# Kernel tuning notes

Hardware: AMD Instinct MI355X
Metric: run time of the kernel (lower is better)

The kernel has to match this reference:

```python
import jax, jax.numpy as jnp
import numpy as np

H = 256
B = 2048
T = 512


def setup_inputs() -> dict:
    key = jax.random.key(0)
    k0, k1, k2, k3, k4 = jax.random.split(key, 5)
    s = 1.0 / np.sqrt(H)  # PyTorch LSTMCell init bound
    return {
        "h": jax.random.normal(k0, (B, H), jnp.float32),
        "W_ih": jax.random.uniform(k1, (4 * H, H), jnp.float32, -s, s),
        "W_hh": jax.random.uniform(k2, (4 * H, H), jnp.float32, -s, s),
        "b_ih": jax.random.uniform(k3, (4 * H,), jnp.float32, -s, s),
        "b_hh": jax.random.uniform(k4, (4 * H,), jnp.float32, -s, s),
        "sequence_length": T,
    }


def _lstm_cell(x, h, c, W_ih, W_hh, b_ih, b_hh):
    # PyTorch LSTMCell: gates ordered (i, f, g, o)
    gates = x @ W_ih.T + h @ W_hh.T + (b_ih + b_hh)  # [B, 4H]
    i, f, g, o = jnp.split(gates, 4, axis=-1)
    i = jax.nn.sigmoid(i)
    f = jax.nn.sigmoid(f)
    g = jnp.tanh(g)
    o = jax.nn.sigmoid(o)
    c2 = f * c + i * g
    h2 = o * jnp.tanh(c2)
    return h2, c2


def reference(h, W_ih, W_hh, b_ih, b_hh, sequence_length):
    b = h.shape[0]
    hid = W_hh.shape[1]
    z = jnp.zeros((b, hid), h.dtype)
    # t == 0: cell(h) with default zero hidden state
    h0, c0 = _lstm_cell(h, z, z, W_ih, W_hh, b_ih, b_hh)

    # t >= 1: input to the cell is the previous hidden output h (linear is None)
    def step(carry, _):
        hh, cc = carry
        h2, c2 = _lstm_cell(hh, hh, cc, W_ih, W_hh, b_ih, b_hh)
        return (h2, c2), h2

    (hf, cf), hs = jax.lax.scan(step, (h0, c0), None, length=sequence_length - 1)
    hs_all = jnp.concatenate([h0[None], hs], axis=0)  # [T, B, H], forward time order
    # predict_backward=True writes x_hat[-t] = h_t, so index 0 stays, rest reversed
    x_hat = jnp.concatenate([hs_all[:1], hs_all[1:][::-1]], axis=0)
    return x_hat, hf, cf
```

## Files before the change

### kernel.cpp

```cpp
#include <hip/hip_runtime.h>

#define HID   256
#define BATCH 2048
#define NGATE 1024
#define BM    16
#define NWG   128
#define TPB   1024
#define LDS_BYTES 147456

typedef __attribute__((ext_vector_type(8))) short bf16x8;
typedef __attribute__((ext_vector_type(4))) float f32x4;

__device__ __forceinline__ unsigned short f2bf(float x){
  unsigned int u = __builtin_bit_cast(unsigned int, x);
  u += 0x7fffu + ((u >> 16) & 1u);
  return (unsigned short)(u >> 16);
}
__device__ __forceinline__ float fsigm(float x){
  return __builtin_amdgcn_rcpf(1.0f + __expf(-x));
}
__device__ __forceinline__ float ftanh_(float x){
  return fmaf(2.0f, __builtin_amdgcn_rcpf(1.0f + __expf(-2.0f*x)), -1.0f);
}

__global__ void pack_kernel(const float* __restrict__ Wih, const float* __restrict__ Whh,
                            const float* __restrict__ bih, const float* __restrict__ bhh,
                            unsigned short* __restrict__ Wih_p,
                            unsigned short* __restrict__ Wsum_p,
                            float* __restrict__ bias){
  int tid = blockIdx.x * blockDim.x + threadIdx.x;
  int j  = tid & 7;
  int ln = (tid >> 3) & 63;
  int kt = (tid >> 9) & 7;
  int nt = tid >> 12;
  int n = nt*16 + (ln & 15);
  int k = kt*32 + (ln >> 4)*8 + j;
  float wih = Wih[n*HID + k];
  float whh = Whh[n*HID + k];
  Wih_p[tid]  = f2bf(wih);
  Wsum_p[tid] = f2bf(wih + whh);
  if (tid < NGATE) bias[tid] = bih[tid] + bhh[tid];
}

template<bool FIRST>
__device__ __forceinline__ void lstm_step(
    int t, int T, int g, int w, int l, int l15, int lq,
    const unsigned short* __restrict__ hcur,
    unsigned short* __restrict__ hnext,
    const unsigned short* __restrict__ wl,
    const bf16x8 (&wregs)[4][4],
    const unsigned short* __restrict__ Wih_p,
    const unsigned short* __restrict__ Wsum_p,
    const float (&bv)[4], float (&cs)[4],
    float* __restrict__ out)
{
  const f32x4 z = {0.f,0.f,0.f,0.f};
  f32x4 acc[4] = {z,z,z,z};

  if constexpr (FIRST){
    #pragma unroll
    for (int kt = 0; kt < 8; ++kt){
      bf16x8 av = *(const bf16x8*)&hcur[kt*512 + l*8];
      #pragma unroll
      for (int ga = 0; ga < 4; ++ga){
        bf16x8 bfr = *(const bf16x8*)(Wih_p + (size_t)((ga*16 + w)*8 + kt)*512 + l*8);
        acc[ga] = __builtin_amdgcn_mfma_f32_16x16x32_bf16(av, bfr, acc[ga], 0, 0, 0);
      }
    }
  } else {
    bf16x8 bs[4][2];
    #pragma unroll
    for (int ks = 0; ks < 2; ++ks)
      #pragma unroll
      for (int ga = 0; ga < 4; ++ga)
        bs[ga][ks] = *(const bf16x8*)(Wsum_p + (size_t)((ga*16 + w)*8 + 6 + ks)*512 + l*8);
    __builtin_amdgcn_sched_barrier(0);

    #pragma unroll
    for (int kc = 0; kc < 4; ++kc){
      bf16x8 av = *(const bf16x8*)&hcur[kc*512 + l*8];
      #pragma unroll
      for (int ga = 0; ga < 4; ++ga)
        acc[ga] = __builtin_amdgcn_mfma_f32_16x16x32_bf16(av, wregs[ga][kc], acc[ga], 0, 0, 0);
    }

    #pragma unroll
    for (int kc = 0; kc < 2; ++kc){
      bf16x8 av = *(const bf16x8*)&hcur[(4+kc)*512 + l*8];
      #pragma unroll
      for (int ga = 0; ga < 4; ++ga){
        bf16x8 bfr = *(const bf16x8*)&wl[((w*8) + ga*2 + kc)*512 + l*8];
        acc[ga] = __builtin_amdgcn_mfma_f32_16x16x32_bf16(av, bfr, acc[ga], 0, 0, 0);
      }
    }

    #pragma unroll
    for (int ks = 0; ks < 2; ++ks){
      bf16x8 av = *(const bf16x8*)&hcur[(6+ks)*512 + l*8];
      #pragma unroll
      for (int ga = 0; ga < 4; ++ga)
        acc[ga] = __builtin_amdgcn_mfma_f32_16x16x32_bf16(av, bs[ga][ks], acc[ga], 0, 0, 0);
    }
  }

  const int u   = w*16 + l15;
  const int ktu = w >> 1;
  const int kgu = ((w & 1) << 1) | (l15 >> 3);
  const int ju  = l15 & 7;
  const int orow = FIRST ? 0 : (T - t);
  float* __restrict__ orp = out + (size_t)orow * (BATCH*HID);
  const bool last = (t == T - 1);

  #pragma unroll
  for (int r = 0; r < 4; ++r){
    const int m = lq*4 + r;
    const float iv = fsigm (acc[0][r] + bv[0]);
    const float fv = fsigm (acc[1][r] + bv[1]);
    const float gv = ftanh_(acc[2][r] + bv[2]);
    const float ov = fsigm (acc[3][r] + bv[3]);
    const float cn = fv * cs[r] + iv * gv;
    cs[r] = cn;
    const float hv = ov * ftanh_(cn);
    hnext[ktu*512 + (kgu*16 + m)*8 + ju] = f2bf(hv);
    const size_t gi = (size_t)(g*BM + m)*HID + u;
    orp[gi] = hv;
    if (last){
      out[(size_t)T*(BATCH*HID) + gi]       = hv;
      out[(size_t)(T + 1)*(BATCH*HID) + gi] = cn;
    }
  }
}

__global__ __launch_bounds__(TPB, 4)
void lstm_kernel(const float* __restrict__ h_in,
                 const unsigned short* __restrict__ Wih_p,
                 const unsigned short* __restrict__ Wsum_p,
                 const float* __restrict__ bias,
                 const int* __restrict__ seqlen,
                 float* __restrict__ out){
  extern __shared__ unsigned short lds[];
  unsigned short* hb = lds;
  unsigned short* wl = lds + 8192;

  const int T   = seqlen[0];
  const int g   = blockIdx.x;
  const int tid = threadIdx.x;
  const int w   = tid >> 6;
  const int l   = tid & 63;
  const int l15 = l & 15;
  const int lq  = l >> 4;
  const int u   = w*16 + l15;

  float bv[4];
  #pragma unroll
  for (int ga = 0; ga < 4; ++ga) bv[ga] = bias[ga*256 + u];

  bf16x8 wregs[4][4];
  #pragma unroll
  for (int ga = 0; ga < 4; ++ga)
    #pragma unroll
    for (int kc = 0; kc < 4; ++kc)
      wregs[ga][kc] = *(const bf16x8*)(Wsum_p + (size_t)((ga*16 + w)*8 + kc)*512 + l*8);

  #pragma unroll
  for (int ga = 0; ga < 4; ++ga)
    #pragma unroll
    for (int kc = 0; kc < 2; ++kc)
      *(bf16x8*)&wl[((w*8) + ga*2 + kc)*512 + l*8] =
        *(const bf16x8*)(Wsum_p + (size_t)((ga*16 + w)*8 + 4 + kc)*512 + l*8);

  {
    const int ktu = w >> 1;
    const int kgu = ((w & 1) << 1) | (l15 >> 3);
    const int ju  = l15 & 7;
    #pragma unroll
    for (int r = 0; r < 4; ++r){
      const int m = lq*4 + r;
      hb[ktu*512 + (kgu*16 + m)*8 + ju] = f2bf(h_in[(size_t)(g*BM + m)*HID + u]);
    }
  }

  float cs[4] = {0.f, 0.f, 0.f, 0.f};
  __syncthreads();

  lstm_step<true>(0, T, g, w, l, l15, lq, hb, hb + 4096, wl, wregs, Wih_p, Wsum_p, bv, cs, out);
  __syncthreads();
  int buf = 1;
  for (int t = 1; t < T; ++t){
    lstm_step<false>(t, T, g, w, l, l15, lq,
                     hb + buf*4096, hb + (buf^1)*4096, wl, wregs, Wih_p, Wsum_p, bv, cs, out);
    __syncthreads();
    buf ^= 1;
  }
}

extern "C" void kernel_launch(void* const* d_in, const int* in_sizes, int n_in,
                              void* d_out, int out_size, void* d_ws, size_t ws_size,
                              hipStream_t stream) {
  const float* h_in = (const float*)d_in[0];
  const float* Wih  = (const float*)d_in[1];
  const float* Whh  = (const float*)d_in[2];
  const float* bih  = (const float*)d_in[3];
  const float* bhh  = (const float*)d_in[4];
  const int*   seq  = (const int*)  d_in[5];
  float* out = (float*)d_out;

  unsigned short* Wih_p  = (unsigned short*)d_ws;
  unsigned short* Wsum_p = Wih_p + (size_t)NGATE * HID;
  float*          bias   = (float*)(Wsum_p + (size_t)NGATE * HID);

  static bool attr_set = false;
  if (!attr_set){
    hipFuncSetAttribute((const void*)lstm_kernel,
                        hipFuncAttributeMaxDynamicSharedMemorySize, LDS_BYTES);
    attr_set = true;
  }

  pack_kernel<<<dim3((NGATE*HID)/256), dim3(256), 0, stream>>>(
      Wih, Whh, bih, bhh, Wih_p, Wsum_p, bias);

  lstm_kernel<<<dim3(NWG), dim3(TPB), LDS_BYTES, stream>>>(
      h_in, Wih_p, Wsum_p, bias, seq, out);
}
```

Baseline: 2.690 ms.

## Halve workgroup to 8 waves, each computing two unit tiles with more register-resident weights

Workgroups shrink from 16 to 8 waves, and each wave now owns 32 hidden units (two 16-wide tiles) per gate. More of the summed weight matrix stays in VGPRs (28 fragments), a larger slice goes to LDS, and the rest is streamed from global memory in staged batches between MFMA groups. Bias is folded into the accumulator initialisation, and __syncthreads is replaced by an explicit lgkmcnt wait plus s_barrier. The aim is cheaper per-step barriers and fewer global weight reloads, at the cost of half as many waves to hide latency and higher register pressure.

```diff
diff --git a/kernel.cpp b/kernel.cpp
--- a/kernel.cpp
+++ b/kernel.cpp
@@ -5,8 +5,8 @@
 #define NGATE 1024
 #define BM    16
 #define NWG   128
-#define TPB   1024
-#define LDS_BYTES 147456
+#define TPB   512
+#define LDS_BYTES 163840
 
 typedef __attribute__((ext_vector_type(8))) short bf16x8;
 typedef __attribute__((ext_vector_type(4))) float f32x4;
@@ -22,6 +22,15 @@
 __device__ __forceinline__ float ftanh_(float x){
   return fmaf(2.0f, __builtin_amdgcn_rcpf(1.0f + __expf(-2.0f*x)), -1.0f);
 }
+
+#define MFMA(a,b,c) __builtin_amdgcn_mfma_f32_16x16x32_bf16((a),(b),(c),0,0,0)
+
+#define STEP_BARRIER() do {                                   \
+    __builtin_amdgcn_sched_barrier(0);                        \
+    asm volatile("s_waitcnt lgkmcnt(0)" ::: "memory");        \
+    __builtin_amdgcn_s_barrier();                             \
+    __builtin_amdgcn_sched_barrier(0);                        \
+  } while (0)
 
 __global__ void pack_kernel(const float* __restrict__ Wih, const float* __restrict__ Whh,
                             const float* __restrict__ bih, const float* __restrict__ bhh,
@@ -42,96 +51,7 @@
   if (tid < NGATE) bias[tid] = bih[tid] + bhh[tid];
 }
 
-template<bool FIRST>
-__device__ __forceinline__ void lstm_step(
-    int t, int T, int g, int w, int l, int l15, int lq,
-    const unsigned short* __restrict__ hcur,
-    unsigned short* __restrict__ hnext,
-    const unsigned short* __restrict__ wl,
-    const bf16x8 (&wregs)[4][4],
-    const unsigned short* __restrict__ Wih_p,
-    const unsigned short* __restrict__ Wsum_p,
-    const float (&bv)[4], float (&cs)[4],
-    float* __restrict__ out)
-{
-  const f32x4 z = {0.f,0.f,0.f,0.f};
-  f32x4 acc[4] = {z,z,z,z};
-
-  if constexpr (FIRST){
-    #pragma unroll
-    for (int kt = 0; kt < 8; ++kt){
-      bf16x8 av = *(const bf16x8*)&hcur[kt*512 + l*8];
-      #pragma unroll
-      for (int ga = 0; ga < 4; ++ga){
-        bf16x8 bfr = *(const bf16x8*)(Wih_p + (size_t)((ga*16 + w)*8 + kt)*512 + l*8);
-        acc[ga] = __builtin_amdgcn_mfma_f32_16x16x32_bf16(av, bfr, acc[ga], 0, 0, 0);
-      }
-    }
-  } else {
-    bf16x8 bs[4][2];
-    #pragma unroll
-    for (int ks = 0; ks < 2; ++ks)
-      #pragma unroll
-      for (int ga = 0; ga < 4; ++ga)
-        bs[ga][ks] = *(const bf16x8*)(Wsum_p + (size_t)((ga*16 + w)*8 + 6 + ks)*512 + l*8);
-    __builtin_amdgcn_sched_barrier(0);
-
-    #pragma unroll
-    for (int kc = 0; kc < 4; ++kc){
-      bf16x8 av = *(const bf16x8*)&hcur[kc*512 + l*8];
-      #pragma unroll
-      for (int ga = 0; ga < 4; ++ga)
-        acc[ga] = __builtin_amdgcn_mfma_f32_16x16x32_bf16(av, wregs[ga][kc], acc[ga], 0, 0, 0);
-    }
-
-    #pragma unroll
-    for (int kc = 0; kc < 2; ++kc){
-      bf16x8 av = *(const bf16x8*)&hcur[(4+kc)*512 + l*8];
-      #pragma unroll
-      for (int ga = 0; ga < 4; ++ga){
-        bf16x8 bfr = *(const bf16x8*)&wl[((w*8) + ga*2 + kc)*512 + l*8];
-        acc[ga] = __builtin_amdgcn_mfma_f32_16x16x32_bf16(av, bfr, acc[ga], 0, 0, 0);
-      }
-    }
-
-    #pragma unroll
-    for (int ks = 0; ks < 2; ++ks){
-      bf16x8 av = *(const bf16x8*)&hcur[(6+ks)*512 + l*8];
-      #pragma unroll
-      for (int ga = 0; ga < 4; ++ga)
-        acc[ga] = __builtin_amdgcn_mfma_f32_16x16x32_bf16(av, bs[ga][ks], acc[ga], 0, 0, 0);
-    }
-  }
-
-  const int u   = w*16 + l15;
-  const int ktu = w >> 1;
-  const int kgu = ((w & 1) << 1) | (l15 >> 3);
-  const int ju  = l15 & 7;
-  const int orow = FIRST ? 0 : (T - t);
-  float* __restrict__ orp = out + (size_t)orow * (BATCH*HID);
-  const bool last = (t == T - 1);
-
-  #pragma unroll
-  for (int r = 0; r < 4; ++r){
-    const int m = lq*4 + r;
-    const float iv = fsigm (acc[0][r] + bv[0]);
-    const float fv = fsigm (acc[1][r] + bv[1]);
-    const float gv = ftanh_(acc[2][r] + bv[2]);
-    const float ov = fsigm (acc[3][r] + bv[3]);
-    const float cn = fv * cs[r] + iv * gv;
-    cs[r] = cn;
-    const float hv = ov * ftanh_(cn);
-    hnext[ktu*512 + (kgu*16 + m)*8 + ju] = f2bf(hv);
-    const size_t gi = (size_t)(g*BM + m)*HID + u;
-    orp[gi] = hv;
-    if (last){
-      out[(size_t)T*(BATCH*HID) + gi]       = hv;
-      out[(size_t)(T + 1)*(BATCH*HID) + gi] = cn;
-    }
-  }
-}
-
-__global__ __launch_bounds__(TPB, 4)
+__global__ __launch_bounds__(TPB, 2)
 void lstm_kernel(const float* __restrict__ h_in,
                  const unsigned short* __restrict__ Wih_p,
                  const unsigned short* __restrict__ Wsum_p,
@@ -149,47 +69,225 @@
   const int l   = tid & 63;
   const int l15 = l & 15;
   const int lq  = l >> 4;
-  const int u   = w*16 + l15;
-
-  float bv[4];
-  #pragma unroll
-  for (int ga = 0; ga < 4; ++ga) bv[ga] = bias[ga*256 + u];
-
-  bf16x8 wregs[4][4];
+
+  auto WOFF = [&](int ga, int ut, int kt) -> size_t {
+    return ((size_t)((ga*16 + w*2 + ut)*8 + kt))*512 + (size_t)l*8;
+  };
+
+  float bv[4][2];
   #pragma unroll
   for (int ga = 0; ga < 4; ++ga)
     #pragma unroll
-    for (int kc = 0; kc < 4; ++kc)
-      wregs[ga][kc] = *(const bf16x8*)(Wsum_p + (size_t)((ga*16 + w)*8 + kc)*512 + l*8);
-
+    for (int ut = 0; ut < 2; ++ut)
+      bv[ga][ut] = bias[ga*256 + w*32 + ut*16 + l15];
+
+  bf16x8 wr[28];
+  #pragma unroll
+  for (int kt = 0; kt < 3; ++kt)
+    #pragma unroll
+    for (int ga = 0; ga < 4; ++ga)
+      #pragma unroll
+      for (int ut = 0; ut < 2; ++ut)
+        wr[kt*8 + ga*2 + ut] = *(const bf16x8*)(Wsum_p + WOFF(ga, ut, kt));
+  #pragma unroll
+  for (int ga = 0; ga < 2; ++ga)
+    #pragma unroll
+    for (int ut = 0; ut < 2; ++ut)
+      wr[24 + ga*2 + ut] = *(const bf16x8*)(Wsum_p + WOFF(ga, ut, 3));
+  #pragma unroll
+  for (int i = 0; i < 28; ++i) asm volatile("" : "+v"(wr[i]));
+
+  #pragma unroll
+  for (int ga = 2; ga < 4; ++ga)
+    #pragma unroll
+    for (int ut = 0; ut < 2; ++ut)
+      *(bf16x8*)&wl[((w*18) + (ga-2)*2 + ut)*512 + l*8] =
+        *(const bf16x8*)(Wsum_p + WOFF(ga, ut, 3));
   #pragma unroll
   for (int ga = 0; ga < 4; ++ga)
     #pragma unroll
-    for (int kc = 0; kc < 2; ++kc)
-      *(bf16x8*)&wl[((w*8) + ga*2 + kc)*512 + l*8] =
-        *(const bf16x8*)(Wsum_p + (size_t)((ga*16 + w)*8 + 4 + kc)*512 + l*8);
-
-  {
-    const int ktu = w >> 1;
-    const int kgu = ((w & 1) << 1) | (l15 >> 3);
-    const int ju  = l15 & 7;
+    for (int ut = 0; ut < 2; ++ut)
+      *(bf16x8*)&wl[((w*18) + 4 + ga*2 + ut)*512 + l*8] =
+        *(const bf16x8*)(Wsum_p + WOFF(ga, ut, 4));
+  #pragma unroll
+  for (int ga = 0; ga < 3; ++ga)
+    #pragma unroll
+    for (int ut = 0; ut < 2; ++ut)
+      *(bf16x8*)&wl[((w*18) + 12 + ga*2 + ut)*512 + l*8] =
+        *(const bf16x8*)(Wsum_p + WOFF(ga, ut, 5));
+
+  #pragma unroll
+  for (int ut = 0; ut < 2; ++ut){
+    const int u   = w*32 + ut*16 + l15;
+    const int kgu = (u & 31) >> 3;
+    const int ju  = u & 7;
     #pragma unroll
     for (int r = 0; r < 4; ++r){
       const int m = lq*4 + r;
-      hb[ktu*512 + (kgu*16 + m)*8 + ju] = f2bf(h_in[(size_t)(g*BM + m)*HID + u]);
+      hb[w*512 + (kgu*16 + m)*8 + ju] = f2bf(h_in[(size_t)(g*BM + m)*HID + u]);
     }
   }
 
-  float cs[4] = {0.f, 0.f, 0.f, 0.f};
+  float cs[2][4];
+  #pragma unroll
+  for (int ut = 0; ut < 2; ++ut)
+    #pragma unroll
+    for (int r = 0; r < 4; ++r) cs[ut][r] = 0.0f;
+
   __syncthreads();
 
-  lstm_step<true>(0, T, g, w, l, l15, lq, hb, hb + 4096, wl, wregs, Wih_p, Wsum_p, bv, cs, out);
-  __syncthreads();
+  auto step = [&](int t, const unsigned short* __restrict__ hcur,
+                  unsigned short* __restrict__ hnext, bool first){
+    f32x4 acc[4][2];
+    #pragma unroll
+    for (int ga = 0; ga < 4; ++ga)
+      #pragma unroll
+      for (int ut = 0; ut < 2; ++ut){
+        acc[ga][ut][0] = bv[ga][ut]; acc[ga][ut][1] = bv[ga][ut];
+        acc[ga][ut][2] = bv[ga][ut]; acc[ga][ut][3] = bv[ga][ut];
+      }
+
+    if (first){
+      #pragma unroll 1
+      for (int kt = 0; kt < 8; ++kt){
+        bf16x8 av = *(const bf16x8*)&hcur[kt*512 + l*8];
+        #pragma unroll
+        for (int ga = 0; ga < 4; ++ga)
+          #pragma unroll
+          for (int ut = 0; ut < 2; ++ut){
+            bf16x8 bfr = *(const bf16x8*)(Wih_p + WOFF(ga, ut, kt));
+            acc[ga][ut] = MFMA(av, bfr, acc[ga][ut]);
+          }
+      }
+    } else {
+      bf16x8 sA[4];
+      sA[0] = *(const bf16x8*)(Wsum_p + WOFF(3, 0, 5));
+      sA[1] = *(const bf16x8*)(Wsum_p + WOFF(3, 1, 5));
+      sA[2] = *(const bf16x8*)(Wsum_p + WOFF(0, 0, 6));
+      sA[3] = *(const bf16x8*)(Wsum_p + WOFF(0, 1, 6));
+      __builtin_amdgcn_sched_barrier(0);
+
+      #pragma unroll
+      for (int kt = 0; kt < 3; ++kt){
+        bf16x8 av = *(const bf16x8*)&hcur[kt*512 + l*8];
+        #pragma unroll
+        for (int ga = 0; ga < 4; ++ga)
+          #pragma unroll
+          for (int ut = 0; ut < 2; ++ut)
+            acc[ga][ut] = MFMA(av, wr[kt*8 + ga*2 + ut], acc[ga][ut]);
+      }
+
+      bf16x8 sB[6];
+      #pragma unroll
+      for (int ga = 1; ga < 4; ++ga)
+        #pragma unroll
+        for (int ut = 0; ut < 2; ++ut)
+          sB[(ga-1)*2 + ut] = *(const bf16x8*)(Wsum_p + WOFF(ga, ut, 6));
+      __builtin_amdgcn_sched_barrier(0);
+
+      {
+        bf16x8 av = *(const bf16x8*)&hcur[3*512 + l*8];
+        #pragma unroll
+        for (int ga = 0; ga < 2; ++ga)
+          #pragma unroll
+          for (int ut = 0; ut < 2; ++ut)
+            acc[ga][ut] = MFMA(av, wr[24 + ga*2 + ut], acc[ga][ut]);
+        #pragma unroll
+        for (int ga = 2; ga < 4; ++ga)
+          #pragma unroll
+          for (int ut = 0; ut < 2; ++ut){
+            bf16x8 bfr = *(const bf16x8*)&wl[((w*18) + (ga-2)*2 + ut)*512 + l*8];
+            acc[ga][ut] = MFMA(av, bfr, acc[ga][ut]);
+          }
+      }
+      {
+        bf16x8 av = *(const bf16x8*)&hcur[4*512 + l*8];
+        #pragma unroll
+        for (int ga = 0; ga < 4; ++ga)
+          #pragma unroll
+          for (int ut = 0; ut < 2; ++ut){
+            bf16x8 bfr = *(const bf16x8*)&wl[((w*18) + 4 + ga*2 + ut)*512 + l*8];
+            acc[ga][ut] = MFMA(av, bfr, acc[ga][ut]);
+          }
+      }
+
+      bf16x8 sC[8];
+      #pragma unroll
+      for (int ga = 0; ga < 4; ++ga)
+        #pragma unroll
+        for (int ut = 0; ut < 2; ++ut)
+          sC[ga*2 + ut] = *(const bf16x8*)(Wsum_p + WOFF(ga, ut, 7));
+      __builtin_amdgcn_sched_barrier(0);
+
+      {
+        bf16x8 av = *(const bf16x8*)&hcur[5*512 + l*8];
+        #pragma unroll
+        for (int ga = 0; ga < 3; ++ga)
+          #pragma unroll
+          for (int ut = 0; ut < 2; ++ut){
+            bf16x8 bfr = *(const bf16x8*)&wl[((w*18) + 12 + ga*2 + ut)*512 + l*8];
+            acc[ga][ut] = MFMA(av, bfr, acc[ga][ut]);
+          }
+        acc[3][0] = MFMA(av, sA[0], acc[3][0]);
+        acc[3][1] = MFMA(av, sA[1], acc[3][1]);
+      }
+      {
+        bf16x8 av = *(const bf16x8*)&hcur[6*512 + l*8];
+        acc[0][0] = MFMA(av, sA[2], acc[0][0]);
+        acc[0][1] = MFMA(av, sA[3], acc[0][1]);
+        #pragma unroll
+        for (int ga = 1; ga < 4; ++ga)
+          #pragma unroll
+          for (int ut = 0; ut < 2; ++ut)
+            acc[ga][ut] = MFMA(av, sB[(ga-1)*2 + ut], acc[ga][ut]);
+      }
+      {
+        bf16x8 av = *(const bf16x8*)&hcur[7*512 + l*8];
+        #pragma unroll
+        for (int ga = 0; ga < 4; ++ga)
+          #pragma unroll
+          for (int ut = 0; ut < 2; ++ut)
+            acc[ga][ut] = MFMA(av, sC[ga*2 + ut], acc[ga][ut]);
+      }
+    }
+
+    const int orow = first ? 0 : (T - t);
+    float* __restrict__ orp = out + (size_t)orow * (BATCH*HID);
+    const bool last = (t == T - 1);
+
+    #pragma unroll
+    for (int ut = 0; ut < 2; ++ut){
+      const int u   = w*32 + ut*16 + l15;
+      const int kgu = (u & 31) >> 3;
+      const int ju  = u & 7;
+      #pragma unroll
+      for (int r = 0; r < 4; ++r){
+        const int m = lq*4 + r;
+        const float iv = fsigm (acc[0][ut][r]);
+        const float fv = fsigm (acc[1][ut][r]);
+        const float gv = ftanh_(acc[2][ut][r]);
+        const float ov = fsigm (acc[3][ut][r]);
+        const float cn = fv * cs[ut][r] + iv * gv;
+        cs[ut][r] = cn;
+        const float hv = ov * ftanh_(cn);
+        hnext[w*512 + (kgu*16 + m)*8 + ju] = f2bf(hv);
+        const size_t gi = (size_t)(g*BM + m)*HID + u;
+        orp[gi] = hv;
+        if (last){
+          out[(size_t)T*(BATCH*HID) + gi]       = hv;
+          out[(size_t)(T + 1)*(BATCH*HID) + gi] = cn;
+        }
+      }
+    }
+  };
+
+  step(0, hb, hb + 4096, true);
+  STEP_BARRIER();
   int buf = 1;
+  #pragma unroll 1
   for (int t = 1; t < T; ++t){
-    lstm_step<false>(t, T, g, w, l, l15, lq,
-                     hb + buf*4096, hb + (buf^1)*4096, wl, wregs, Wih_p, Wsum_p, bv, cs, out);
-    __syncthreads();
+    step(t, hb + buf*4096, hb + (buf^1)*4096, false);
+    STEP_BARRIER();
     buf ^= 1;
   }
 }
```

After: 3.387 ms. 1.26x slower.
